# Kernel optimization log

Measured on AMD Instinct MI355X. Metric: run time of the kernel, lower is better.

## Reference

```python
import jax, jax.numpy as jnp
import numpy as np

ALPHA = 40.0
BETA = 20.0
NUM_INSTANCES = 8  # samples per class in the PK-sampled batch


def setup_inputs() -> dict:
    key = jax.random.key(0)
    n, d = 4096, 1024
    x = jax.random.normal(key, (n, d), dtype=jnp.float32)
    # L2-normalize embeddings (standard for this loss; margins 0.8/1.1 assume dist in [0,2])
    inputs = x / jnp.linalg.norm(x, axis=1, keepdims=True)
    targets = (jnp.arange(n) // NUM_INSTANCES).astype(jnp.int32)
    return {"inputs": inputs, "targets": targets}


def reference(inputs, targets):
    n = inputs.shape[0]
    # euclidean_dist: ||xi||^2 + ||xj||^2 - 2 xi.xj, clamp, sqrt
    sq = jnp.sum(inputs * inputs, axis=1)  # [n]
    dist = sq[:, None] + sq[None, :] - 2.0 * (inputs @ inputs.T)
    dist = jnp.sqrt(jnp.clip(dist, 1e-12, None))  # [n, n]

    same = targets[:, None] == targets[None, :]
    eye = jnp.eye(n, dtype=bool)
    pos_mask = same & ~eye   # positives excluding self
    neg_mask = ~same         # negatives

    exp_a = jnp.exp(ALPHA * (1.0 - dist))
    pos_logit = jnp.sum(jnp.where(pos_mask, exp_a, 0.0), axis=1)  # [n]
    neg_logit = jnp.sum(jnp.where(neg_mask, exp_a, 0.0), axis=1)  # [n]
    # a_lr is computed from .data in the original (detached)
    a_lr = jax.lax.stop_gradient(1.0 - pos_logit / (pos_logit + neg_logit))

    pos_loss = jnp.log(jnp.sum(jnp.where(pos_mask, jnp.exp(BETA * (dist - 0.8)), 0.0), axis=1))
    neg_loss = jnp.log(jnp.sum(jnp.where(neg_mask, jnp.exp(BETA * (1.1 - dist)), 0.0), axis=1))
    loss = jnp.mean(a_lr * (pos_loss + neg_loss))

    # acc_num never incremented in the original -> accuracy == 0
    accuracy = jnp.zeros((), dtype=jnp.float32)
    pos_d = jax.lax.stop_gradient(
        jnp.sum(jnp.where(pos_mask, dist, 0.0)) / jnp.sum(pos_mask))
    neg_d = jax.lax.stop_gradient(
        jnp.sum(jnp.where(neg_mask, dist, 0.0)) / jnp.sum(neg_mask))
    return jnp.stack([loss, accuracy, pos_d, neg_d])  # [4]
```

## Files before the change

kernel.cpp:

```cpp
#include <hip/hip_runtime.h>

#define N 4096
#define D 1024
#define BM 128
#define BN 128
#define BK 64
#define NSLOT 32

typedef __bf16 bf16x8 __attribute__((ext_vector_type(8)));
typedef float floatx4 __attribute__((ext_vector_type(4)));

__device__ __forceinline__ ushort f2bf(float f) {
    union { float f; uint32_t u; } c; c.f = f;
    uint32_t u = c.u;
    uint32_t r = u + 0x7FFFu + ((u >> 16) & 1u);
    return (ushort)(r >> 16);
}

__global__ __launch_bounds__(256) void prep_kernel(const float* __restrict__ x,
                                                   ushort* __restrict__ xb,
                                                   float* __restrict__ sq,
                                                   float* __restrict__ out) {
    if (blockIdx.x == 0 && threadIdx.x == 0) {
        out[0] = 0.f; out[1] = 0.f; out[2] = 0.f; out[3] = 0.f;
    }
    int row = blockIdx.x * 4 + (threadIdx.x >> 6);
    int lane = threadIdx.x & 63;
    const float4* xr = (const float4*)(x + (size_t)row * D);
    ushort4* br = (ushort4*)(xb + (size_t)row * D);
    float s = 0.f;
    #pragma unroll
    for (int j = 0; j < 4; ++j) {
        float4 v = xr[j * 64 + lane];
        s += v.x * v.x + v.y * v.y + v.z * v.z + v.w * v.w;
        br[j * 64 + lane] = make_ushort4(f2bf(v.x), f2bf(v.y), f2bf(v.z), f2bf(v.w));
    }
    #pragma unroll
    for (int sh = 1; sh < 64; sh <<= 1) s += __shfl_xor(s, sh);
    if (lane == 0) sq[row] = s;
}

__global__ __launch_bounds__(256, 2) void gemm_fused(const ushort* __restrict__ xb,
                                                     const float* __restrict__ sq,
                                                     float* __restrict__ colPart) {
    __shared__ ushort smem[2 * BM * BK];

    const int bi = blockIdx.y, bj = blockIdx.x;
    const int i0 = bi * BM, j0 = bj * BN;
    const int tid = threadIdx.x;
    const int lane = tid & 63, wave = tid >> 6;
    const int wm = wave >> 1, wn = wave & 1;
    const int quad = lane >> 4, c16 = lane & 15;

    int goff[8];
    #pragma unroll
    for (int it = 0; it < 8; ++it) {
        int chunk = it * 256 + tid;
        int half = chunk >> 10;
        int c = chunk & 1023;
        int g = c >> 7, p = c & 127;
        int r = p >> 3;
        int kc = ((p & 7) - (r >> 1)) & 7;
        int grow = (half ? j0 : i0) + g * 16 + r;
        goff[it] = grow * D + kc * 8;
    }

    floatx4 acc[4][4];
    #pragma unroll
    for (int a = 0; a < 4; ++a)
        #pragma unroll
        for (int b = 0; b < 4; ++b) acc[a][b] = (floatx4){0.f, 0.f, 0.f, 0.f};

    for (int kt = 0; kt < D; kt += BK) {
        #pragma unroll
        for (int it = 0; it < 8; ++it) {
            const ushort* gp = xb + goff[it] + kt;
            ushort* lp = smem + (it * 256 + tid) * 8;
            __builtin_amdgcn_global_load_lds(
                (const __attribute__((address_space(1))) void*)gp,
                (__attribute__((address_space(3))) void*)lp, 16, 0, 0);
        }
        __syncthreads();

        #pragma unroll
        for (int s = 0; s < 2; ++s) {
            const int fs = (c16 << 3) | ((4 * s + quad + (c16 >> 1)) & 7);
            bf16x8 afrag[4], bfrag[4];
            #pragma unroll
            for (int t = 0; t < 4; ++t) {
                afrag[t] = *(const bf16x8*)(smem + (wm * 4 + t) * 1024 + fs * 8);
                bfrag[t] = *(const bf16x8*)(smem + 8192 + (wn * 4 + t) * 1024 + fs * 8);
            }
            #pragma unroll
            for (int tm = 0; tm < 4; ++tm)
                #pragma unroll
                for (int tn = 0; tn < 4; ++tn)
                    acc[tm][tn] = __builtin_amdgcn_mfma_f32_16x16x32_bf16(
                        afrag[tm], bfrag[tn], acc[tm][tn], 0, 0, 0);
        }
        __syncthreads();
    }

    float sqi[4][4];
    #pragma unroll
    for (int tm = 0; tm < 4; ++tm)
        #pragma unroll
        for (int r = 0; r < 4; ++r)
            sqi[tm][r] = sq[i0 + wm * 64 + tm * 16 + quad * 4 + r];
    float sqj[4];
    #pragma unroll
    for (int tn = 0; tn < 4; ++tn)
        sqj[tn] = sq[j0 + wn * 64 + tn * 16 + c16];

    float cpa[4], cna[4], cpb[4], cnb[4], cpd[4], cnd[4];
    const bool diag = (bi == bj);

    #pragma unroll
    for (int tn = 0; tn < 4; ++tn) {
        float pa = 0.f, na = 0.f, pb = 0.f, nb = 0.f, pd = 0.f, nd = 0.f;
        if (!diag) {
            #pragma unroll
            for (int tm = 0; tm < 4; ++tm)
                #pragma unroll
                for (int r = 0; r < 4; ++r) {
                    float dot = acc[tm][tn][r];
                    float dsq = sqi[tm][r] + sqj[tn] - 2.0f * dot;
                    float dist = sqrtf(fmaxf(dsq, 1e-12f));
                    float t = __expf(20.0f * (1.1f - dist));
                    na = fmaf(t, t, na);
                    nb += t;
                    nd += dist;
                }
        } else {
            const int gj = j0 + wn * 64 + tn * 16 + c16;
            const int gjc = gj >> 3;
            #pragma unroll
            for (int tm = 0; tm < 4; ++tm)
                #pragma unroll
                for (int r = 0; r < 4; ++r) {
                    const int gi = i0 + wm * 64 + tm * 16 + quad * 4 + r;
                    float dot = acc[tm][tn][r];
                    float dsq = sqi[tm][r] + sqj[tn] - 2.0f * dot;
                    float dist = sqrtf(fmaxf(dsq, 1e-12f));
                    float t = __expf(20.0f * (1.1f - dist));
                    bool same = (gi >> 3) == gjc;
                    if (same) {
                        if (gi != gj) {
                            pa = fmaf(t, t, pa);
                            pb += __expf(20.0f * (dist - 0.8f));
                            pd += dist;
                        }
                    } else {
                        na = fmaf(t, t, na);
                        nb += t;
                        nd += dist;
                    }
                }
        }
        cpa[tn] = pa; cna[tn] = na; cpb[tn] = pb;
        cnb[tn] = nb; cpd[tn] = pd; cnd[tn] = nd;
    }

    #pragma unroll
    for (int tn = 0; tn < 4; ++tn) {
        #pragma unroll
        for (int s = 16; s < 64; s <<= 1) {
            cna[tn] += __shfl_xor(cna[tn], s);
            cnb[tn] += __shfl_xor(cnb[tn], s);
            cnd[tn] += __shfl_xor(cnd[tn], s);
        }
        if (diag) {
            #pragma unroll
            for (int s = 16; s < 64; s <<= 1) {
                cpa[tn] += __shfl_xor(cpa[tn], s);
                cpb[tn] += __shfl_xor(cpb[tn], s);
                cpd[tn] += __shfl_xor(cpd[tn], s);
            }
        }
    }

    float* colBuf = (float*)smem;
    #pragma unroll
    for (int tn = 0; tn < 4; ++tn) {
        int cb = (wm * 128 + wn * 64 + tn * 16 + c16) * 6;
        colBuf[cb + 0] = cpa[tn]; colBuf[cb + 1] = cna[tn];
        colBuf[cb + 2] = cpb[tn]; colBuf[cb + 3] = cnb[tn];
        colBuf[cb + 4] = cpd[tn]; colBuf[cb + 5] = cnd[tn];
    }
    __syncthreads();

    float* dst = colPart + (size_t)bi * N * 6 + (size_t)j0 * 6;
    #pragma unroll
    for (int it = 0; it < 3; ++it) {
        int idx = it * 256 + tid;
        dst[idx] = colBuf[idx] + colBuf[768 + idx];
    }
}

__global__ __launch_bounds__(256) void reduce_finalize(const float* __restrict__ colPart,
                                                       float* __restrict__ out) {
    int j = blockIdx.x * 256 + threadIdx.x;
    float pa = 0.f, na = 0.f, pb = 0.f, nb = 0.f, pd = 0.f, nd = 0.f;
    for (int s = 0; s < NSLOT; ++s) {
        const float* p = colPart + (size_t)s * N * 6 + (size_t)j * 6;
        pa += p[0]; na += p[1]; pb += p[2];
        nb += p[3]; pd += p[4]; nd += p[5];
    }
    float a_lr = 1.0f - pa / (pa + na);
    float L = a_lr * (logf(pb) + logf(nb));

    #pragma unroll
    for (int s = 1; s < 64; s <<= 1) {
        L  += __shfl_xor(L, s);
        pd += __shfl_xor(pd, s);
        nd += __shfl_xor(nd, s);
    }
    __shared__ float r0[4], r1[4], r2[4];
    int lane = threadIdx.x & 63, w = threadIdx.x >> 6;
    if (lane == 0) { r0[w] = L; r1[w] = pd; r2[w] = nd; }
    __syncthreads();
    if (threadIdx.x == 0) {
        float Ls = r0[0] + r0[1] + r0[2] + r0[3];
        float Ps = r1[0] + r1[1] + r1[2] + r1[3];
        float Gs = r2[0] + r2[1] + r2[2] + r2[3];
        atomicAdd(out + 0, Ls / (float)N);
        atomicAdd(out + 2, Ps / ((float)N * 7.0f));
        atomicAdd(out + 3, Gs / ((float)N * (float)(N - 8)));
    }
}

extern "C" void kernel_launch(void* const* d_in, const int* in_sizes, int n_in,
                              void* d_out, int out_size, void* d_ws, size_t ws_size,
                              hipStream_t stream) {
    const float* x = (const float*)d_in[0];
    float* out = (float*)d_out;
    char* ws = (char*)d_ws;

    ushort* xb      = (ushort*)ws;
    float*  sq      = (float*)(ws + (size_t)N * D * 2);
    float*  colPart = (float*)(ws + (size_t)N * D * 2 + N * 4);

    prep_kernel<<<N / 4, 256, 0, stream>>>(x, xb, sq, out);

    dim3 grid(N / BN, N / BM);
    gemm_fused<<<grid, 256, 0, stream>>>(xb, sq, colPart);

    reduce_finalize<<<N / 256, 256, 0, stream>>>(colPart, out);
}
```

Before: 108.8 us.

## Quantize embeddings to scaled FP8 and use FP8 MFMA for the Gram matrix

Converts the normalized embeddings to FP8 (scaled by 32) instead of bf16, halving the bytes loaded per K step and doubling K per tile, and switches the MFMA to the fp8 variant. The LDS swizzle and fragment addressing are reworked for 16-byte FP8 chunks, and the scale is folded back into the distance computation. This cuts memory traffic and raises matrix throughput, but FP8 rounding error in the dot products is amplified by exp(40*(1-dist)), which risks accuracy.

```diff
diff --git a/kernel.cpp b/kernel.cpp
--- a/kernel.cpp
+++ b/kernel.cpp
@@ -4,21 +4,14 @@
 #define D 1024
 #define BM 128
 #define BN 128
-#define BK 64
+#define BKB 128
 #define NSLOT 32
 
-typedef __bf16 bf16x8 __attribute__((ext_vector_type(8)));
 typedef float floatx4 __attribute__((ext_vector_type(4)));
-
-__device__ __forceinline__ ushort f2bf(float f) {
-    union { float f; uint32_t u; } c; c.f = f;
-    uint32_t u = c.u;
-    uint32_t r = u + 0x7FFFu + ((u >> 16) & 1u);
-    return (ushort)(r >> 16);
-}
+typedef long long i64;
 
 __global__ __launch_bounds__(256) void prep_kernel(const float* __restrict__ x,
-                                                   ushort* __restrict__ xb,
+                                                   unsigned char* __restrict__ xq,
                                                    float* __restrict__ sq,
                                                    float* __restrict__ out) {
     if (blockIdx.x == 0 && threadIdx.x == 0) {
@@ -27,23 +20,25 @@
     int row = blockIdx.x * 4 + (threadIdx.x >> 6);
     int lane = threadIdx.x & 63;
     const float4* xr = (const float4*)(x + (size_t)row * D);
-    ushort4* br = (ushort4*)(xb + (size_t)row * D);
+    unsigned int* qr = (unsigned int*)(xq + (size_t)row * D);
     float s = 0.f;
     #pragma unroll
     for (int j = 0; j < 4; ++j) {
         float4 v = xr[j * 64 + lane];
         s += v.x * v.x + v.y * v.y + v.z * v.z + v.w * v.w;
-        br[j * 64 + lane] = make_ushort4(f2bf(v.x), f2bf(v.y), f2bf(v.z), f2bf(v.w));
+        unsigned int w = __builtin_amdgcn_cvt_pk_fp8_f32(v.x * 32.f, v.y * 32.f, 0, false);
+        w = __builtin_amdgcn_cvt_pk_fp8_f32(v.z * 32.f, v.w * 32.f, w, true);
+        qr[j * 64 + lane] = w;
     }
     #pragma unroll
     for (int sh = 1; sh < 64; sh <<= 1) s += __shfl_xor(s, sh);
     if (lane == 0) sq[row] = s;
 }
 
-__global__ __launch_bounds__(256, 2) void gemm_fused(const ushort* __restrict__ xb,
+__global__ __launch_bounds__(256, 2) void gemm_fused(const unsigned char* __restrict__ xq,
                                                      const float* __restrict__ sq,
                                                      float* __restrict__ colPart) {
-    __shared__ ushort smem[2 * BM * BK];
+    __shared__ __align__(16) unsigned char smem[2 * BM * BKB];
 
     const int bi = blockIdx.y, bj = blockIdx.x;
     const int i0 = bi * BM, j0 = bj * BN;
@@ -60,9 +55,9 @@
         int c = chunk & 1023;
         int g = c >> 7, p = c & 127;
         int r = p >> 3;
-        int kc = ((p & 7) - (r >> 1)) & 7;
+        int kc = ((p & 7) - (r & 7)) & 7;
         int grow = (half ? j0 : i0) + g * 16 + r;
-        goff[it] = grow * D + kc * 8;
+        goff[it] = grow * D + kc * 16;
     }
 
     floatx4 acc[4][4];
@@ -71,11 +66,11 @@
         #pragma unroll
         for (int b = 0; b < 4; ++b) acc[a][b] = (floatx4){0.f, 0.f, 0.f, 0.f};
 
-    for (int kt = 0; kt < D; kt += BK) {
+    for (int kt = 0; kt < D; kt += BKB) {
         #pragma unroll
         for (int it = 0; it < 8; ++it) {
-            const ushort* gp = xb + goff[it] + kt;
-            ushort* lp = smem + (it * 256 + tid) * 8;
+            const unsigned char* gp = xq + goff[it] + kt;
+            unsigned char* lp = smem + (it * 256 + tid) * 16;
             __builtin_amdgcn_global_load_lds(
                 (const __attribute__((address_space(1))) void*)gp,
                 (__attribute__((address_space(3))) void*)lp, 16, 0, 0);
@@ -83,19 +78,21 @@
         __syncthreads();
 
         #pragma unroll
-        for (int s = 0; s < 2; ++s) {
-            const int fs = (c16 << 3) | ((4 * s + quad + (c16 >> 1)) & 7);
-            bf16x8 afrag[4], bfrag[4];
+        for (int s = 0; s < 4; ++s) {
+            const int kc16 = 2 * s + (quad >> 1);
+            const int sub = quad & 1;
+            const int fb = ((kc16 + (c16 & 7)) & 7) * 16 + sub * 8 + c16 * 128;
+            i64 afrag[4], bfrag[4];
             #pragma unroll
             for (int t = 0; t < 4; ++t) {
-                afrag[t] = *(const bf16x8*)(smem + (wm * 4 + t) * 1024 + fs * 8);
-                bfrag[t] = *(const bf16x8*)(smem + 8192 + (wn * 4 + t) * 1024 + fs * 8);
+                afrag[t] = *(const i64*)(smem + (wm * 4 + t) * 2048 + fb);
+                bfrag[t] = *(const i64*)(smem + 16384 + (wn * 4 + t) * 2048 + fb);
             }
             #pragma unroll
             for (int tm = 0; tm < 4; ++tm)
                 #pragma unroll
                 for (int tn = 0; tn < 4; ++tn)
-                    acc[tm][tn] = __builtin_amdgcn_mfma_f32_16x16x32_bf16(
+                    acc[tm][tn] = __builtin_amdgcn_mfma_f32_16x16x32_fp8_fp8(
                         afrag[tm], bfrag[tn], acc[tm][tn], 0, 0, 0);
         }
         __syncthreads();
@@ -114,6 +111,7 @@
 
     float cpa[4], cna[4], cpb[4], cnb[4], cpd[4], cnd[4];
     const bool diag = (bi == bj);
+    const float DS = -0.001953125f;
 
     #pragma unroll
     for (int tn = 0; tn < 4; ++tn) {
@@ -124,7 +122,7 @@
                 #pragma unroll
                 for (int r = 0; r < 4; ++r) {
                     float dot = acc[tm][tn][r];
-                    float dsq = sqi[tm][r] + sqj[tn] - 2.0f * dot;
+                    float dsq = fmaf(dot, DS, sqi[tm][r] + sqj[tn]);
                     float dist = sqrtf(fmaxf(dsq, 1e-12f));
                     float t = __expf(20.0f * (1.1f - dist));
                     na = fmaf(t, t, na);
@@ -140,7 +138,7 @@
                 for (int r = 0; r < 4; ++r) {
                     const int gi = i0 + wm * 64 + tm * 16 + quad * 4 + r;
                     float dot = acc[tm][tn][r];
-                    float dsq = sqi[tm][r] + sqj[tn] - 2.0f * dot;
+                    float dsq = fmaf(dot, DS, sqi[tm][r] + sqj[tn]);
                     float dist = sqrtf(fmaxf(dsq, 1e-12f));
                     float t = __expf(20.0f * (1.1f - dist));
                     bool same = (gi >> 3) == gjc;
@@ -236,14 +234,14 @@
     float* out = (float*)d_out;
     char* ws = (char*)d_ws;
 
-    ushort* xb      = (ushort*)ws;
-    float*  sq      = (float*)(ws + (size_t)N * D * 2);
-    float*  colPart = (float*)(ws + (size_t)N * D * 2 + N * 4);
-
-    prep_kernel<<<N / 4, 256, 0, stream>>>(x, xb, sq, out);
+    unsigned char* xq = (unsigned char*)ws;
+    float* sq         = (float*)(ws + (size_t)N * D);
+    float* colPart    = (float*)(ws + (size_t)N * D + N * 4);
+
+    prep_kernel<<<N / 4, 256, 0, stream>>>(x, xq, sq, out);
 
     dim3 grid(N / BN, N / BM);
-    gemm_fused<<<grid, 256, 0, stream>>>(xb, sq, colPart);
+    gemm_fused<<<grid, 256, 0, stream>>>(xq, sq, colPart);
 
     reduce_finalize<<<N / 256, 256, 0, stream>>>(colPart, out);
 }
```

Result: faster. 103.9 us (-4.4%).
